# Performance work log

Hardware: AMD Instinct MI355X
Metric: run time of the kernel (lower is better)

The kernel has to match this reference:

```python
import jax, jax.numpy as jnp
import numpy as np

B_, L_, D_, H_ = 2, 1024, 1024, 16


def _matrixR(L, d_model):
    # Transformer-XL sinusoid table, reversed along the position axis (reverse=True)
    inv_freq = 1.0 / (10000.0 ** (np.arange(0, d_model, 2, dtype=np.float32) / d_model))
    sinus = np.arange(L, dtype=np.float32)[:, None] * inv_freq[None, :]
    mat = np.zeros((L, d_model), dtype=np.float32)
    mat[:, 0::2] = np.sin(sinus)
    mat[:, 1::2] = np.cos(sinus)
    return jnp.asarray(mat[::-1].copy())


def _shift_b(x):
    # x: (b, h, L, L) -> TXL relative shift + lower-triangular mask
    b, h, L, _ = x.shape
    pad = jnp.concatenate([jnp.zeros((b, h, L, 1), x.dtype), x], axis=-1)  # (b,h,L,L+1)
    shifted = pad.reshape(b, h, L + 1, L)[:, :, 1:, :]                      # (b,h,L,L)
    return jnp.tril(shifted)


def setup_inputs() -> dict:
    key = jax.random.key(0)
    ks = jax.random.split(key, 8)
    s = 1.0 / np.sqrt(D_)
    return {
        "E": jax.random.normal(ks[0], (B_, L_, D_), dtype=jnp.float32),
        "Ev": jax.random.normal(ks[1], (B_, L_, D_), dtype=jnp.float32),
        "R": _matrixR(L_, D_),
        "Wq": jax.random.normal(ks[2], (D_, D_), dtype=jnp.float32) * s,
        "Wke": jax.random.normal(ks[3], (D_, D_), dtype=jnp.float32) * s,
        "Wkr": jax.random.normal(ks[4], (D_, D_), dtype=jnp.float32) * s,
        "Wv": jax.random.normal(ks[5], (D_, D_), dtype=jnp.float32) * s,
        "cb": jnp.ones((D_,), dtype=jnp.float32),
        "pb": jnp.ones((D_,), dtype=jnp.float32),
        "Wo_w": jax.random.normal(ks[6], (D_, D_), dtype=jnp.float32) * s,
        "Wo_b": jnp.zeros((D_,), dtype=jnp.float32),
        "ln_g": jnp.ones((D_,), dtype=jnp.float32),
        "ln_b": jnp.zeros((D_,), dtype=jnp.float32),
    }


def reference(E, Ev, R, Wq, Wke, Wkr, Wv, cb, pb, Wo_w, Wo_b, ln_g, ln_b):
    b, L, d = E.shape
    h = H_
    dh = d // h
    # projections -> (b, h, L, dh)
    q = (E @ Wq).reshape(b, L, h, dh).transpose(0, 2, 1, 3)
    k = (Ev @ Wke).reshape(b, L, h, dh).transpose(0, 2, 1, 3)
    v = (Ev @ Wv).reshape(b, L, h, dh).transpose(0, 2, 1, 3)
    # relative-position keys (batch independent): (h, L, dh)
    Q = (R @ Wkr).reshape(L, h, dh).transpose(1, 0, 2)
    # (a) content-content
    A_a = jnp.einsum('bhid,bhjd->bhij', q, k)
    # (b) content-position, with shift trick
    A_b = _shift_b(jnp.einsum('bhid,hjd->bhij', q, Q))
    # (c) global content bias (same for every query row)
    A_c = jnp.einsum('hd,bhjd->bhj', cb.reshape(h, dh), k)[:, :, None, :]  # (b,h,1,L)
    # (d) global position bias (batch independent), shifted
    d_row = jnp.einsum('hd,hjd->hj', pb.reshape(h, dh), Q)                 # (h,L)
    A_d = _shift_b(jnp.broadcast_to(d_row[None, :, None, :], (1, h, L, L)))
    A = A_a + A_b + A_c + A_d
    p = jax.nn.softmax(A, axis=-1)
    Oh = jnp.einsum('bhij,bhjd->bhid', p, v)
    O = Oh.transpose(0, 2, 1, 3).reshape(b, L, d)
    # residual + output proj (dropout is identity in eval) + LayerNorm
    res = Ev + (O @ Wo_w + Wo_b)
    mu = jnp.mean(res, axis=-1, keepdims=True)
    var = jnp.mean((res - mu) ** 2, axis=-1, keepdims=True)
    return (res - mu) * jax.lax.rsqrt(var + 1e-5) * ln_g + ln_b
```

## Files before the change

### kernel.cpp

```cpp
#include <hip/hip_runtime.h>
#include <hip/hip_bf16.h>
#include <math.h>

#define B_ 2
#define L_ 1024
#define D_ 1024
#define H_ 16

typedef short short8 __attribute__((ext_vector_type(8)));
typedef float f32x4  __attribute__((ext_vector_type(4)));

__device__ __forceinline__ short f2bf(float f) {
  unsigned u = __float_as_uint(f);
  u += 0x7fff + ((u >> 16) & 1);
  return (short)(u >> 16);
}
__device__ __forceinline__ float bf2f(short s) {
  return __uint_as_float(((unsigned)(unsigned short)s) << 16);
}
__device__ __forceinline__ int swz(int row, int slot) {
  return row * 64 + ((slot ^ (row & 7)) << 3);
}

template<int A_BF16, int OUT_F32>
__device__ __forceinline__ void mm128_body(const void* Ap, const short* Bt,
                                           void* Cp, int N, int K,
                                           int bx, int by) {
  __shared__ short As[8192];
  __shared__ short Bs[8192];
  const int tid = threadIdx.x;
  const int l = tid & 63, w = tid >> 6;
  const int row0 = by * 128, col0 = bx * 128;
  const int wm = (w >> 1) * 64, wn = (w & 1) * 64;
  const f32x4 fz = {0.f, 0.f, 0.f, 0.f};

  f32x4 acc[4][4];
  #pragma unroll
  for (int i = 0; i < 4; ++i)
    #pragma unroll
    for (int j = 0; j < 4; ++j) acc[i][j] = fz;

  int crow[4], cslot[4];
  #pragma unroll
  for (int c = 0; c < 4; ++c) { int ci = tid + c * 256; crow[c] = ci >> 3; cslot[c] = ci & 7; }

  float4 af[4][2];
  short8 ab[4];
  short8 bb[4];

  auto loadT = [&](int k0) {
    #pragma unroll
    for (int c = 0; c < 4; ++c) {
      if (A_BF16) {
        ab[c] = *(const short8*)&((const short*)Ap)[(size_t)(row0 + crow[c]) * K + k0 + cslot[c] * 8];
      } else {
        const float* ap = &((const float*)Ap)[(size_t)(row0 + crow[c]) * K + k0 + cslot[c] * 8];
        af[c][0] = *(const float4*)ap;
        af[c][1] = *(const float4*)(ap + 4);
      }
      bb[c] = *(const short8*)&Bt[(size_t)(col0 + crow[c]) * K + k0 + cslot[c] * 8];
    }
  };
  auto writeT = [&]() {
    #pragma unroll
    for (int c = 0; c < 4; ++c) {
      short8 av;
      if (A_BF16) {
        av = ab[c];
      } else {
        av[0] = f2bf(af[c][0].x); av[1] = f2bf(af[c][0].y);
        av[2] = f2bf(af[c][0].z); av[3] = f2bf(af[c][0].w);
        av[4] = f2bf(af[c][1].x); av[5] = f2bf(af[c][1].y);
        av[6] = f2bf(af[c][1].z); av[7] = f2bf(af[c][1].w);
      }
      *(short8*)&As[swz(crow[c], cslot[c])] = av;
      *(short8*)&Bs[swz(crow[c], cslot[c])] = bb[c];
    }
  };

  const int nt = K / 64;
  loadT(0); writeT(); __syncthreads();

  for (int t = 0; t < nt; ++t) {
    if (t + 1 < nt) loadT((t + 1) * 64);
    #pragma unroll
    for (int kf = 0; kf < 2; ++kf) {
      short8 a[4], b[4];
      #pragma unroll
      for (int mf = 0; mf < 4; ++mf)
        a[mf] = *(const short8*)&As[swz(wm + mf * 16 + (l & 15), kf * 4 + (l >> 4))];
      #pragma unroll
      for (int nf = 0; nf < 4; ++nf)
        b[nf] = *(const short8*)&Bs[swz(wn + nf * 16 + (l & 15), kf * 4 + (l >> 4))];
      #pragma unroll
      for (int mf = 0; mf < 4; ++mf)
        #pragma unroll
        for (int nf = 0; nf < 4; ++nf)
          acc[mf][nf] = __builtin_amdgcn_mfma_f32_16x16x32_bf16(a[mf], b[nf], acc[mf][nf], 0, 0, 0);
    }
    if (t + 1 < nt) { __syncthreads(); writeT(); __syncthreads(); }
  }

  #pragma unroll
  for (int mf = 0; mf < 4; ++mf)
    #pragma unroll
    for (int nf = 0; nf < 4; ++nf)
      #pragma unroll
      for (int r = 0; r < 4; ++r) {
        int row = row0 + wm + mf * 16 + (l >> 4) * 4 + r;
        int col = col0 + wn + nf * 16 + (l & 15);
        if (OUT_F32) ((float*)Cp)[(size_t)row * N + col] = acc[mf][nf][r];
        else         ((short*)Cp)[(size_t)row * N + col] = f2bf(acc[mf][nf][r]);
      }
}

__global__ __launch_bounds__(256) void proj_mfma(
    const float* __restrict__ E, const float* __restrict__ Ev, const float* __restrict__ R,
    const short* __restrict__ Wt,
    short* __restrict__ qb, short* __restrict__ kb,
    short* __restrict__ vb, short* __restrict__ Qpb) {
  const int z = blockIdx.z;
  const void* A; const short* Bt; void* C; int M;
  const size_t MM = (size_t)D_ * D_;
  if (z == 0)      { A = E;  Bt = Wt;          C = qb;  M = B_ * L_; }
  else if (z == 1) { A = Ev; Bt = Wt + MM;     C = kb;  M = B_ * L_; }
  else if (z == 2) { A = Ev; Bt = Wt + 3 * MM; C = vb;  M = B_ * L_; }
  else             { A = R;  Bt = Wt + 2 * MM; C = Qpb; M = L_;      }
  if ((int)blockIdx.y * 128 >= M) return;
  mm128_body<0, 0>(A, Bt, C, D_, D_, blockIdx.x, blockIdx.y);
}

__global__ __launch_bounds__(256) void out_mfma(
    const short* __restrict__ Ob, const short* __restrict__ Wot, float* __restrict__ proj) {
  mm128_body<1, 1>(Ob, Wot, proj, D_, D_, blockIdx.x, blockIdx.y);
}

__global__ __launch_bounds__(256) void tcast(
    const float* __restrict__ W0, const float* __restrict__ W1,
    const float* __restrict__ W2, const float* __restrict__ W3,
    const float* __restrict__ W4, short* __restrict__ out) {
  const int z = blockIdx.z;
  const float* W = (z == 0) ? W0 : (z == 1) ? W1 : (z == 2) ? W2 : (z == 3) ? W3 : W4;
  short* Wt = out + (size_t)z * D_ * D_;
  __shared__ short t[64][65];
  const int tid = threadIdx.x;
  const int r0 = blockIdx.y * 64, c0 = blockIdx.x * 64;
  #pragma unroll
  for (int i = 0; i < 4; ++i) {
    int idx = tid + i * 256;
    int r = idx >> 4, c4 = (idx & 15) * 4;
    float4 v = *(const float4*)&W[(size_t)(r0 + r) * D_ + c0 + c4];
    t[c4 + 0][r] = f2bf(v.x); t[c4 + 1][r] = f2bf(v.y);
    t[c4 + 2][r] = f2bf(v.z); t[c4 + 3][r] = f2bf(v.w);
  }
  __syncthreads();
  #pragma unroll
  for (int i = 0; i < 2; ++i) {
    int idx = tid + i * 256;
    int rr = idx >> 3, cc = (idx & 7) * 8;
    short8 o;
    #pragma unroll
    for (int e = 0; e < 8; ++e) o[e] = t[rr][cc + e];
    *(short8*)&Wt[(size_t)(c0 + rr) * D_ + r0 + cc] = o;
  }
}

__global__ __launch_bounds__(256) void cdvec(
    const short* __restrict__ kb, const short* __restrict__ Qpb,
    const float* __restrict__ cb, const float* __restrict__ pb,
    float* __restrict__ cvec, float* __restrict__ dvec) {
  int idx = blockIdx.x * 256 + threadIdx.x;
  if (idx < B_ * H_ * L_) {
    int b = idx >> 14, h = (idx >> 10) & 15, j = idx & 1023;
    const short* kr = &kb[(size_t)(b * L_ + j) * D_ + h * 64];
    const float* cr = &cb[h * 64];
    float s = 0.f;
    #pragma unroll
    for (int d8 = 0; d8 < 8; ++d8) {
      short8 kv = *(const short8*)&kr[d8 * 8];
      #pragma unroll
      for (int e = 0; e < 8; ++e) s += bf2f(kv[e]) * cr[d8 * 8 + e];
    }
    cvec[idx] = s;
  } else {
    int i2 = idx - B_ * H_ * L_;
    if (i2 < H_ * L_) {
      int h = i2 >> 10, m = i2 & 1023;
      const short* qr = &Qpb[(size_t)m * D_ + h * 64];
      const float* pr = &pb[h * 64];
      float s = 0.f;
      #pragma unroll
      for (int d8 = 0; d8 < 8; ++d8) {
        short8 qv = *(const short8*)&qr[d8 * 8];
        #pragma unroll
        for (int e = 0; e < 8; ++e) s += bf2f(qv[e]) * pr[d8 * 8 + e];
      }
      dvec[i2] = s;
    }
  }
}

__global__ __launch_bounds__(256) void attn_mfma(
    const short* __restrict__ qb, const short* __restrict__ kb,
    const short* __restrict__ vb, const short* __restrict__ Qpb,
    const float* __restrict__ cvec, const float* __restrict__ dvec,
    short* __restrict__ Ob) {
  __shared__ short q_s[4096];
  __shared__ short k_s[4096];
  __shared__ short vt_s[4096];
  __shared__ short win_s[8192];
  __shared__ short pb_s[4 * 1312];
  __shared__ float cvec_s[64];
  __shared__ float dvec_s[128];

  const int tid = threadIdx.x;
  const int l = tid & 63, w = tid >> 6;
  const int nib = L_ / 64;
  const int b  = blockIdx.x / (H_ * nib);
  const int hh = (blockIdx.x / nib) % H_;
  const int i0 = (blockIdx.x % nib) * 64;
  const f32x4 fz = {0.f, 0.f, 0.f, 0.f};

  #pragma unroll
  for (int c = 0; c < 2; ++c) {
    int ci = tid + c * 256;
    int r = ci >> 3, s = ci & 7;
    *(short8*)&q_s[swz(r, s)] =
        *(const short8*)&qb[(size_t)(b * L_ + i0 + r) * D_ + hh * 64 + s * 8];
  }
  __syncthreads();

  short8 aq[2];
  {
    int row = w * 16 + (l & 15);
    aq[0] = *(const short8*)&q_s[swz(row, (l >> 4))];
    aq[1] = *(const short8*)&q_s[swz(row, 4 + (l >> 4))];
  }

  float mrow[4], lrow[4];
  f32x4 oacc[4];
  #pragma unroll
  for (int r = 0; r < 4; ++r) { mrow[r] = -3.0e38f; lrow[r] = 0.f; }
  #pragma unroll
  for (int nf = 0; nf < 4; ++nf) oacc[nf] = fz;

  for (int jt = 0; jt < 16; ++jt) {
    const int j0 = jt * 64;
    const bool pos = (j0 <= i0);
    const bool diag = (j0 == i0);
    const int mbase = L_ - 64 - i0 + j0;

    __syncthreads();

    #pragma unroll
    for (int c = 0; c < 2; ++c) {
      int ci = tid + c * 256;
      int r = ci >> 3, s = ci & 7;
      *(short8*)&k_s[swz(r, s)] =
          *(const short8*)&kb[(size_t)(b * L_ + j0 + r) * D_ + hh * 64 + s * 8];
    }
    #pragma unroll
    for (int c = 0; c < 2; ++c) {
      int ci = tid + c * 256;
      int jr = ci >> 3, s = ci & 7;
      short8 vv = *(const short8*)&vb[(size_t)(b * L_ + j0 + jr) * D_ + hh * 64 + s * 8];
      #pragma unroll
      for (int e = 0; e < 8; ++e) {
        int d = s * 8 + e;
        vt_s[d * 64 + (((jr >> 3) ^ (d & 7)) << 3) + (jr & 7)] = vv[e];
      }
    }
    if (tid < 64) cvec_s[tid] = cvec[(size_t)(b * H_ + hh) * L_ + j0 + tid];
    if (pos) {
      #pragma unroll
      for (int c = 0; c < 4; ++c) {
        int ci = tid + c * 256;
        int mm = ci >> 3, s = ci & 7;
        int m = mbase + mm;
        short8 wv = {0, 0, 0, 0, 0, 0, 0, 0};
        if (m < L_) wv = *(const short8*)&Qpb[(size_t)m * D_ + hh * 64 + s * 8];
        *(short8*)&win_s[swz(mm, s)] = wv;
      }
      if (tid < 128) {
        int m = mbase + tid;
        dvec_s[tid] = (m < L_) ? dvec[hh * L_ + m] : 0.f;
      }
    }
    __syncthreads();

    f32x4 sac[4];
    #pragma unroll
    for (int nf = 0; nf < 4; ++nf) sac[nf] = fz;
    #pragma unroll
    for (int kf = 0; kf < 2; ++kf) {
      #pragma unroll
      for (int nf = 0; nf < 4; ++nf) {
        short8 bk = *(const short8*)&k_s[swz(nf * 16 + (l & 15), kf * 4 + (l >> 4))];
        sac[nf] = __builtin_amdgcn_mfma_f32_16x16x32_bf16(aq[kf], bk, sac[nf], 0, 0, 0);
      }
    }

    if (pos) {
      f32x4 pacc[5];
      #pragma unroll
      for (int u = 0; u < 5; ++u) pacc[u] = fz;
      const int nf0 = 3 - w;
      #pragma unroll
      for (int kf = 0; kf < 2; ++kf) {
        #pragma unroll
        for (int u = 0; u < 5; ++u) {
          short8 bw = *(const short8*)&win_s[swz((nf0 + u) * 16 + (l & 15), kf * 4 + (l >> 4))];
          pacc[u] = __builtin_amdgcn_mfma_f32_16x16x32_bf16(aq[kf], bw, pacc[u], 0, 0, 0);
        }
      }
      const int pbb = w * 1312;
      #pragma unroll
      for (int u = 0; u < 5; ++u)
        #pragma unroll
        for (int r = 0; r < 4; ++r) {
          int row = (l >> 4) * 4 + r;
          pb_s[pbb + row * 82 + u * 16 + (l & 15)] = f2bf(pacc[u][r]);
        }
    }

    #pragma unroll
    for (int nf = 0; nf < 4; ++nf)
      #pragma unroll
      for (int r = 0; r < 4; ++r) {
        int rj = nf * 16 + (l & 15);
        float s = sac[nf][r] + cvec_s[rj];
        if (pos) {
          int ris = (l >> 4) * 4 + r;
          int rib = w * 16 + ris;
          if (!diag || rj <= rib) {
            s += bf2f(pb_s[w * 1312 + ris * 82 + (15 - ris + rj)]);
            s += dvec_s[63 - rib + rj];
          }
        }
        sac[nf][r] = s;
      }

    #pragma unroll
    for (int r = 0; r < 4; ++r) {
      float mx = fmaxf(fmaxf(sac[0][r], sac[1][r]), fmaxf(sac[2][r], sac[3][r]));
      #pragma unroll
      for (int off = 1; off < 16; off <<= 1)
        mx = fmaxf(mx, __shfl_xor(mx, off, 64));
      float mn = fmaxf(mrow[r], mx);
      float sc = __expf(mrow[r] - mn);
      mrow[r] = mn;
      float ls = 0.f;
      #pragma unroll
      for (int nf = 0; nf < 4; ++nf) {
        float p = __expf(sac[nf][r] - mn);
        sac[nf][r] = p;
        ls += p;
      }
      #pragma unroll
      for (int off = 1; off < 16; off <<= 1)
        ls += __shfl_xor(ls, off, 64);
      lrow[r] = lrow[r] * sc + ls;
      #pragma unroll
      for (int nf = 0; nf < 4; ++nf) oacc[nf][r] *= sc;
    }

    #pragma unroll
    for (int nf = 0; nf < 4; ++nf)
      #pragma unroll
      for (int r = 0; r < 4; ++r) {
        int row = (l >> 4) * 4 + r;
        int col = nf * 16 + (l & 15);
        pb_s[w * 1312 + row * 64 + (((col >> 3) ^ (row & 7)) << 3) + (col & 7)] = f2bf(sac[nf][r]);
      }

    #pragma unroll
    for (int kf = 0; kf < 2; ++kf) {
      int prow = l & 15;
      short8 ap = *(const short8*)&pb_s[w * 1312 + prow * 64 + (((kf * 4 + (l >> 4)) ^ (prow & 7)) << 3)];
      #pragma unroll
      for (int nf = 0; nf < 4; ++nf) {
        short8 bv = *(const short8*)&vt_s[swz(nf * 16 + (l & 15), kf * 4 + (l >> 4))];
        oacc[nf] = __builtin_amdgcn_mfma_f32_16x16x32_bf16(ap, bv, oacc[nf], 0, 0, 0);
      }
    }
  }

  #pragma unroll
  for (int nf = 0; nf < 4; ++nf)
    #pragma unroll
    for (int r = 0; r < 4; ++r) {
      int row = i0 + w * 16 + (l >> 4) * 4 + r;
      int col = hh * 64 + nf * 16 + (l & 15);
      Ob[(size_t)(b * L_ + row) * D_ + col] = f2bf(oacc[nf][r] / lrow[r]);
    }
}

__global__ __launch_bounds__(256) void ln_kernel(
    const float* __restrict__ Ev, const float* __restrict__ proj,
    const float* __restrict__ Wo_b, const float* __restrict__ g,
    const float* __restrict__ beta, float* __restrict__ out) {
  const int row = blockIdx.x;
  __shared__ float red[8];
  const int tid = threadIdx.x;
  const int d = tid * 4;

  float4 e  = *(const float4*)&Ev[(size_t)row * D_ + d];
  float4 p  = *(const float4*)&proj[(size_t)row * D_ + d];
  float4 wb = *(const float4*)&Wo_b[d];
  float4 rr = { e.x + p.x + wb.x, e.y + p.y + wb.y,
                e.z + p.z + wb.z, e.w + p.w + wb.w };
  float sum = rr.x + rr.y + rr.z + rr.w;
  float sq  = rr.x * rr.x + rr.y * rr.y + rr.z * rr.z + rr.w * rr.w;

  #pragma unroll
  for (int off = 1; off < 64; off <<= 1) {
    sum += __shfl_xor(sum, off, 64);
    sq  += __shfl_xor(sq,  off, 64);
  }
  const int wid = tid >> 6;
  if ((tid & 63) == 0) { red[wid * 2] = sum; red[wid * 2 + 1] = sq; }
  __syncthreads();
  sum = red[0] + red[2] + red[4] + red[6];
  sq  = red[1] + red[3] + red[5] + red[7];

  const float mu   = sum * (1.f / (float)D_);
  const float var  = sq * (1.f / (float)D_) - mu * mu;
  const float rstd = rsqrtf(var + 1e-5f);

  float4 gg = *(const float4*)&g[d];
  float4 bb = *(const float4*)&beta[d];
  float4 o = { (rr.x - mu) * rstd * gg.x + bb.x,
               (rr.y - mu) * rstd * gg.y + bb.y,
               (rr.z - mu) * rstd * gg.z + bb.z,
               (rr.w - mu) * rstd * gg.w + bb.w };
  *(float4*)&out[(size_t)row * D_ + d] = o;
}

extern "C" void kernel_launch(void* const* d_in, const int* in_sizes, int n_in,
                              void* d_out, int out_size, void* d_ws, size_t ws_size,
                              hipStream_t stream) {
  const float* E    = (const float*)d_in[0];
  const float* Ev   = (const float*)d_in[1];
  const float* R    = (const float*)d_in[2];
  const float* Wq   = (const float*)d_in[3];
  const float* Wke  = (const float*)d_in[4];
  const float* Wkr  = (const float*)d_in[5];
  const float* Wv   = (const float*)d_in[6];
  const float* cb   = (const float*)d_in[7];
  const float* pb   = (const float*)d_in[8];
  const float* Wo_w = (const float*)d_in[9];
  const float* Wo_b = (const float*)d_in[10];
  const float* ln_g = (const float*)d_in[11];
  const float* ln_b = (const float*)d_in[12];
  float* out = (float*)d_out;

  short* qb   = (short*)d_ws;
  short* kb   = qb + 2097152;
  short* vb   = kb + 2097152;
  short* Qpb  = vb + 2097152;
  short* Wt   = Qpb + 1048576;
  short* Ob   = Wt + 5242880;
  float* proj = (float*)(Ob + 2097152);
  float* cvec = proj + 2097152;
  float* dvec = cvec + 32768;

  tcast<<<dim3(16, 16, 5), 256, 0, stream>>>(Wq, Wke, Wkr, Wv, Wo_w, Wt);

  proj_mfma<<<dim3(8, 16, 4), 256, 0, stream>>>(E, Ev, R, Wt, qb, kb, vb, Qpb);

  cdvec<<<192, 256, 0, stream>>>(kb, Qpb, cb, pb, cvec, dvec);

  attn_mfma<<<B_ * H_ * (L_ / 64), 256, 0, stream>>>(qb, kb, vb, Qpb, cvec, dvec, Ob);

  out_mfma<<<dim3(8, 16), 256, 0, stream>>>(Ob, Wt + 4 * (size_t)D_ * D_, proj);

  ln_kernel<<<B_ * L_, 256, 0, stream>>>(Ev, proj, Wo_b, ln_g, ln_b, out);
}
```

Baseline: 240.0 us.

## Pre-cast activations to bf16, use direct-to-LDS GEMM loads, prefetch attention tiles

A new kernel casts E, Ev and R to bf16 up front, so the projection GEMM reads bf16 operands. Both GEMMs now load tiles straight into LDS with global_load_lds instead of staging through registers. The LDS tiles lose their XOR swizzle and the GEMM loop loses its register double-buffering, which risks bank conflicts and exposed load latency. The attention kernel prefetches the next K/V/positional window tile into registers during compute, uses a new V-transpose swizzle, and multiplies by a reciprocal in the epilogue. Workspace buffers are reused by aliasing proj and cvec onto the cast buffers.

```diff
diff --git a/kernel.cpp b/kernel.cpp
--- a/kernel.cpp
+++ b/kernel.cpp
@@ -21,11 +21,36 @@
 __device__ __forceinline__ int swz(int row, int slot) {
   return row * 64 + ((slot ^ (row & 7)) << 3);
 }
-
-template<int A_BF16, int OUT_F32>
-__device__ __forceinline__ void mm128_body(const void* Ap, const short* Bt,
-                                           void* Cp, int N, int K,
-                                           int bx, int by) {
+__device__ __forceinline__ int vswz(int d, int j) {
+  return d * 64 + ((((j >> 3) ^ (d & 7) ^ ((d >> 3) & 7)) & 7) << 3) + (j & 7);
+}
+
+__device__ __forceinline__ void glds16(const void* g, void* l) {
+  __builtin_amdgcn_global_load_lds((const __attribute__((address_space(1))) void*)g,
+                                   (__attribute__((address_space(3))) void*)l, 16, 0, 0);
+}
+
+__global__ __launch_bounds__(256) void castbf(
+    const float* __restrict__ E, const float* __restrict__ Ev,
+    const float* __restrict__ R, short* __restrict__ o) {
+  size_t i8 = ((size_t)blockIdx.x * 256 + threadIdx.x) * 8;
+  const float* src; size_t off;
+  if (i8 < 2097152)      { src = E;  off = i8; }
+  else if (i8 < 4194304) { src = Ev; off = i8 - 2097152; }
+  else                   { src = R;  off = i8 - 4194304; }
+  float4 a = *(const float4*)&src[off];
+  float4 b = *(const float4*)&src[off + 4];
+  short8 v;
+  v[0] = f2bf(a.x); v[1] = f2bf(a.y); v[2] = f2bf(a.z); v[3] = f2bf(a.w);
+  v[4] = f2bf(b.x); v[5] = f2bf(b.y); v[6] = f2bf(b.z); v[7] = f2bf(b.w);
+  *(short8*)&o[i8] = v;
+}
+
+template<int OUT_F32>
+__device__ __forceinline__ void mm_glds(const short* __restrict__ A,
+                                        const short* __restrict__ Bt,
+                                        void* Cp, int N, int K,
+                                        int bx, int by) {
   __shared__ short As[8192];
   __shared__ short Bs[8192];
   const int tid = threadIdx.x;
@@ -40,65 +65,34 @@
     #pragma unroll
     for (int j = 0; j < 4; ++j) acc[i][j] = fz;
 
-  int crow[4], cslot[4];
-  #pragma unroll
-  for (int c = 0; c < 4; ++c) { int ci = tid + c * 256; crow[c] = ci >> 3; cslot[c] = ci & 7; }
-
-  float4 af[4][2];
-  short8 ab[4];
-  short8 bb[4];
-
-  auto loadT = [&](int k0) {
+  const int lrow = l >> 3;
+  const int lcol = (l & 7) * 8;
+
+  for (int t = 0; t < K / 64; ++t) {
+    const int k0 = t * 64;
+    if (t) __syncthreads();
     #pragma unroll
     for (int c = 0; c < 4; ++c) {
-      if (A_BF16) {
-        ab[c] = *(const short8*)&((const short*)Ap)[(size_t)(row0 + crow[c]) * K + k0 + cslot[c] * 8];
-      } else {
-        const float* ap = &((const float*)Ap)[(size_t)(row0 + crow[c]) * K + k0 + cslot[c] * 8];
-        af[c][0] = *(const float4*)ap;
-        af[c][1] = *(const float4*)(ap + 4);
-      }
-      bb[c] = *(const short8*)&Bt[(size_t)(col0 + crow[c]) * K + k0 + cslot[c] * 8];
-    }
-  };
-  auto writeT = [&]() {
-    #pragma unroll
-    for (int c = 0; c < 4; ++c) {
-      short8 av;
-      if (A_BF16) {
-        av = ab[c];
-      } else {
-        av[0] = f2bf(af[c][0].x); av[1] = f2bf(af[c][0].y);
-        av[2] = f2bf(af[c][0].z); av[3] = f2bf(af[c][0].w);
-        av[4] = f2bf(af[c][1].x); av[5] = f2bf(af[c][1].y);
-        av[6] = f2bf(af[c][1].z); av[7] = f2bf(af[c][1].w);
-      }
-      *(short8*)&As[swz(crow[c], cslot[c])] = av;
-      *(short8*)&Bs[swz(crow[c], cslot[c])] = bb[c];
-    }
-  };
-
-  const int nt = K / 64;
-  loadT(0); writeT(); __syncthreads();
-
-  for (int t = 0; t < nt; ++t) {
-    if (t + 1 < nt) loadT((t + 1) * 64);
+      const int rr = (w * 4 + c) * 8 + lrow;
+      glds16(&A[(size_t)(row0 + rr) * K + k0 + lcol], &As[(w * 4 + c) * 512]);
+      glds16(&Bt[(size_t)(col0 + rr) * K + k0 + lcol], &Bs[(w * 4 + c) * 512]);
+    }
+    __syncthreads();
     #pragma unroll
     for (int kf = 0; kf < 2; ++kf) {
       short8 a[4], b[4];
       #pragma unroll
       for (int mf = 0; mf < 4; ++mf)
-        a[mf] = *(const short8*)&As[swz(wm + mf * 16 + (l & 15), kf * 4 + (l >> 4))];
+        a[mf] = *(const short8*)&As[(wm + mf * 16 + (l & 15)) * 64 + (kf * 4 + (l >> 4)) * 8];
       #pragma unroll
       for (int nf = 0; nf < 4; ++nf)
-        b[nf] = *(const short8*)&Bs[swz(wn + nf * 16 + (l & 15), kf * 4 + (l >> 4))];
+        b[nf] = *(const short8*)&Bs[(wn + nf * 16 + (l & 15)) * 64 + (kf * 4 + (l >> 4)) * 8];
       #pragma unroll
       for (int mf = 0; mf < 4; ++mf)
         #pragma unroll
         for (int nf = 0; nf < 4; ++nf)
           acc[mf][nf] = __builtin_amdgcn_mfma_f32_16x16x32_bf16(a[mf], b[nf], acc[mf][nf], 0, 0, 0);
     }
-    if (t + 1 < nt) { __syncthreads(); writeT(); __syncthreads(); }
   }
 
   #pragma unroll
@@ -115,24 +109,24 @@
 }
 
 __global__ __launch_bounds__(256) void proj_mfma(
-    const float* __restrict__ E, const float* __restrict__ Ev, const float* __restrict__ R,
-    const short* __restrict__ Wt,
+    const short* __restrict__ Eb, const short* __restrict__ Evb,
+    const short* __restrict__ Rb, const short* __restrict__ Wt,
     short* __restrict__ qb, short* __restrict__ kb,
     short* __restrict__ vb, short* __restrict__ Qpb) {
   const int z = blockIdx.z;
-  const void* A; const short* Bt; void* C; int M;
+  const short* A; const short* Bt; short* C; int M;
   const size_t MM = (size_t)D_ * D_;
-  if (z == 0)      { A = E;  Bt = Wt;          C = qb;  M = B_ * L_; }
-  else if (z == 1) { A = Ev; Bt = Wt + MM;     C = kb;  M = B_ * L_; }
-  else if (z == 2) { A = Ev; Bt = Wt + 3 * MM; C = vb;  M = B_ * L_; }
-  else             { A = R;  Bt = Wt + 2 * MM; C = Qpb; M = L_;      }
+  if (z == 0)      { A = Eb;  Bt = Wt;          C = qb;  M = B_ * L_; }
+  else if (z == 1) { A = Evb; Bt = Wt + MM;     C = kb;  M = B_ * L_; }
+  else if (z == 2) { A = Evb; Bt = Wt + 3 * MM; C = vb;  M = B_ * L_; }
+  else             { A = Rb;  Bt = Wt + 2 * MM; C = Qpb; M = L_;      }
   if ((int)blockIdx.y * 128 >= M) return;
-  mm128_body<0, 0>(A, Bt, C, D_, D_, blockIdx.x, blockIdx.y);
+  mm_glds<0>(A, Bt, C, D_, D_, blockIdx.x, blockIdx.y);
 }
 
 __global__ __launch_bounds__(256) void out_mfma(
     const short* __restrict__ Ob, const short* __restrict__ Wot, float* __restrict__ proj) {
-  mm128_body<1, 1>(Ob, Wot, proj, D_, D_, blockIdx.x, blockIdx.y);
+  mm_glds<1>(Ob, Wot, proj, D_, D_, blockIdx.x, blockIdx.y);
 }
 
 __global__ __launch_bounds__(256) void tcast(
@@ -220,13 +214,75 @@
   const int hh = (blockIdx.x / nib) % H_;
   const int i0 = (blockIdx.x % nib) * 64;
   const f32x4 fz = {0.f, 0.f, 0.f, 0.f};
-
+  const short8 sz = {0, 0, 0, 0, 0, 0, 0, 0};
+
+  short8 rk[2], rv[2], rw[4];
+  float rc = 0.f, rd = 0.f;
+
+  auto stage_load = [&](int jt) {
+    const int j0 = jt * 64;
+    const bool pos = (j0 <= i0);
+    const int mbase = L_ - 64 - i0 + j0;
+    #pragma unroll
+    for (int c = 0; c < 2; ++c) {
+      int ci = tid + c * 256;
+      int r = ci >> 3, s = ci & 7;
+      rk[c] = *(const short8*)&kb[(size_t)(b * L_ + j0 + r) * D_ + hh * 64 + s * 8];
+      rv[c] = *(const short8*)&vb[(size_t)(b * L_ + j0 + r) * D_ + hh * 64 + s * 8];
+    }
+    if (pos) {
+      #pragma unroll
+      for (int c = 0; c < 4; ++c) {
+        int ci = tid + c * 256;
+        int mm = ci >> 3, s = ci & 7;
+        int m = mbase + mm;
+        rw[c] = (m < L_) ? *(const short8*)&Qpb[(size_t)m * D_ + hh * 64 + s * 8] : sz;
+      }
+      if (tid < 128) {
+        int m = mbase + tid;
+        rd = (m < L_) ? dvec[hh * L_ + m] : 0.f;
+      }
+    }
+    if (tid < 64) rc = cvec[(size_t)(b * H_ + hh) * L_ + j0 + tid];
+  };
+
+  auto stage_write = [&](int jt) {
+    const bool pos = (jt * 64 <= i0);
+    #pragma unroll
+    for (int c = 0; c < 2; ++c) {
+      int ci = tid + c * 256;
+      int r = ci >> 3, s = ci & 7;
+      *(short8*)&k_s[swz(r, s)] = rk[c];
+      #pragma unroll
+      for (int e = 0; e < 8; ++e) {
+        int d = s * 8 + e;
+        vt_s[vswz(d, r)] = rv[c][e];
+      }
+    }
+    if (pos) {
+      #pragma unroll
+      for (int c = 0; c < 4; ++c) {
+        int ci = tid + c * 256;
+        int mm = ci >> 3, s = ci & 7;
+        *(short8*)&win_s[swz(mm, s)] = rw[c];
+      }
+      if (tid < 128) dvec_s[tid] = rd;
+    }
+    if (tid < 64) cvec_s[tid] = rc;
+  };
+
+  short8 rq[2];
   #pragma unroll
   for (int c = 0; c < 2; ++c) {
     int ci = tid + c * 256;
     int r = ci >> 3, s = ci & 7;
-    *(short8*)&q_s[swz(r, s)] =
-        *(const short8*)&qb[(size_t)(b * L_ + i0 + r) * D_ + hh * 64 + s * 8];
+    rq[c] = *(const short8*)&qb[(size_t)(b * L_ + i0 + r) * D_ + hh * 64 + s * 8];
+  }
+  stage_load(0);
+  #pragma unroll
+  for (int c = 0; c < 2; ++c) {
+    int ci = tid + c * 256;
+    *(short8*)&q_s[swz(ci >> 3, ci & 7)] = rq[c];
   }
   __syncthreads();
 
@@ -248,45 +304,10 @@
     const int j0 = jt * 64;
     const bool pos = (j0 <= i0);
     const bool diag = (j0 == i0);
-    const int mbase = L_ - 64 - i0 + j0;
-
+
+    stage_write(jt);
     __syncthreads();
-
-    #pragma unroll
-    for (int c = 0; c < 2; ++c) {
-      int ci = tid + c * 256;
-      int r = ci >> 3, s = ci & 7;
-      *(short8*)&k_s[swz(r, s)] =
-          *(const short8*)&kb[(size_t)(b * L_ + j0 + r) * D_ + hh * 64 + s * 8];
-    }
-    #pragma unroll
-    for (int c = 0; c < 2; ++c) {
-      int ci = tid + c * 256;
-      int jr = ci >> 3, s = ci & 7;
-      short8 vv = *(const short8*)&vb[(size_t)(b * L_ + j0 + jr) * D_ + hh * 64 + s * 8];
-      #pragma unroll
-      for (int e = 0; e < 8; ++e) {
-        int d = s * 8 + e;
-        vt_s[d * 64 + (((jr >> 3) ^ (d & 7)) << 3) + (jr & 7)] = vv[e];
-      }
-    }
-    if (tid < 64) cvec_s[tid] = cvec[(size_t)(b * H_ + hh) * L_ + j0 + tid];
-    if (pos) {
-      #pragma unroll
-      for (int c = 0; c < 4; ++c) {
-        int ci = tid + c * 256;
-        int mm = ci >> 3, s = ci & 7;
-        int m = mbase + mm;
-        short8 wv = {0, 0, 0, 0, 0, 0, 0, 0};
-        if (m < L_) wv = *(const short8*)&Qpb[(size_t)m * D_ + hh * 64 + s * 8];
-        *(short8*)&win_s[swz(mm, s)] = wv;
-      }
-      if (tid < 128) {
-        int m = mbase + tid;
-        dvec_s[tid] = (m < L_) ? dvec[hh * L_ + m] : 0.f;
-      }
-    }
-    __syncthreads();
+    if (jt < 15) stage_load(jt + 1);
 
     f32x4 sac[4];
     #pragma unroll
@@ -379,20 +400,23 @@
       short8 ap = *(const short8*)&pb_s[w * 1312 + prow * 64 + (((kf * 4 + (l >> 4)) ^ (prow & 7)) << 3)];
       #pragma unroll
       for (int nf = 0; nf < 4; ++nf) {
-        short8 bv = *(const short8*)&vt_s[swz(nf * 16 + (l & 15), kf * 4 + (l >> 4))];
+        short8 bv = *(const short8*)&vt_s[vswz(nf * 16 + (l & 15), (kf * 4 + (l >> 4)) * 8)];
         oacc[nf] = __builtin_amdgcn_mfma_f32_16x16x32_bf16(ap, bv, oacc[nf], 0, 0, 0);
       }
     }
-  }
-
-  #pragma unroll
-  for (int nf = 0; nf < 4; ++nf)
-    #pragma unroll
-    for (int r = 0; r < 4; ++r) {
+    __syncthreads();
+  }
+
+  #pragma unroll
+  for (int r = 0; r < 4; ++r) {
+    float inv = 1.f / lrow[r];
+    #pragma unroll
+    for (int nf = 0; nf < 4; ++nf) {
       int row = i0 + w * 16 + (l >> 4) * 4 + r;
       int col = hh * 64 + nf * 16 + (l & 15);
-      Ob[(size_t)(b * L_ + row) * D_ + col] = f2bf(oacc[nf][r] / lrow[r]);
-    }
+      Ob[(size_t)(b * L_ + row) * D_ + col] = f2bf(oacc[nf][r] * inv);
+    }
+  }
 }
 
 __global__ __launch_bounds__(256) void ln_kernel(
@@ -454,19 +478,25 @@
   const float* ln_b = (const float*)d_in[12];
   float* out = (float*)d_out;
 
-  short* qb   = (short*)d_ws;
-  short* kb   = qb + 2097152;
-  short* vb   = kb + 2097152;
-  short* Qpb  = vb + 2097152;
-  short* Wt   = Qpb + 1048576;
-  short* Ob   = Wt + 5242880;
-  float* proj = (float*)(Ob + 2097152);
-  float* cvec = proj + 2097152;
+  short* ws   = (short*)d_ws;
+  short* Eb   = ws;
+  short* Evb  = ws + 2097152;
+  short* Rb   = ws + 4194304;
+  short* qb   = ws + 5242880;
+  short* kb   = ws + 7340032;
+  short* vb   = ws + 9437184;
+  short* Qpb  = ws + 11534336;
+  short* Wt   = ws + 12582912;
+  short* Ob   = ws + 17825792;
+  float* proj = (float*)Eb;
+  float* cvec = (float*)Rb;
   float* dvec = cvec + 32768;
 
+  castbf<<<2560, 256, 0, stream>>>(E, Ev, R, Eb);
+
   tcast<<<dim3(16, 16, 5), 256, 0, stream>>>(Wq, Wke, Wkr, Wv, Wo_w, Wt);
 
-  proj_mfma<<<dim3(8, 16, 4), 256, 0, stream>>>(E, Ev, R, Wt, qb, kb, vb, Qpb);
+  proj_mfma<<<dim3(8, 16, 4), 256, 0, stream>>>(Eb, Evb, Rb, Wt, qb, kb, vb, Qpb);
 
   cdvec<<<192, 256, 0, stream>>>(kb, Qpb, cb, pb, cvec, dvec);
 
```

New measurement: 227.0 us. 1.06x faster.
